# Kernel optimization log

Measured on AMD Instinct MI355X. Metric: run time of the kernel, lower is better.

Reference implementation:

```python
import jax, jax.numpy as jnp
import numpy as np

B, S, E, H = 2, 2048, 1024, 16
DH = E // H


def setup_inputs() -> dict:
    key = jax.random.key(0)
    ks = jax.random.split(key, 9)
    s = 1.0 / np.sqrt(E)
    return {
        "queries": jax.random.normal(ks[0], (B, S, E), dtype=jnp.float32),
        "keys": jax.random.normal(ks[1], (B, S, E), dtype=jnp.float32),
        "values": jax.random.normal(ks[2], (B, S, E), dtype=jnp.float32),
        "mask": jax.random.randint(ks[3], (B, 1, 1, S), 0, 2, dtype=jnp.int32),
        "Wq": jax.random.normal(ks[4], (E, E), dtype=jnp.float32) * s,
        "Wk": jax.random.normal(ks[5], (E, E), dtype=jnp.float32) * s,
        "Wv": jax.random.normal(ks[6], (E, E), dtype=jnp.float32) * s,
        "Wo": jax.random.normal(ks[7], (E, E), dtype=jnp.float32) * s,
        "bo": jax.random.normal(ks[8], (E,), dtype=jnp.float32) * s,
    }


def reference(queries, keys, values, mask, Wq, Wk, Wv, Wo, bo):
    n, d_q, _ = queries.shape
    d_k = keys.shape[1]
    # Linear projections (torch Linear: x @ W.T), then split into heads
    q = (queries @ Wq.T).reshape(n, d_q, H, DH)
    k = (keys @ Wk.T).reshape(n, d_k, H, DH)
    v = (values @ Wv.T).reshape(n, d_k, H, DH)
    # [n, H, d_q, d_k] attention scores
    energy = jnp.einsum("nqhd,nkhd->nhqk", q, k)
    energy = jnp.where(mask == 0, jnp.float32(-1e20), energy)
    # NOTE: original scales by sqrt(key seq length), not head dim -- kept faithful
    attn = jax.nn.softmax(energy / jnp.sqrt(jnp.float32(d_k)), axis=3)
    out = jnp.einsum("nhql,nlhd->nqhd", attn, v).reshape(n, d_q, E)
    return out @ Wo.T + bo
```

## Files before the change

kernel.cpp:

```cpp
#include <hip/hip_runtime.h>
#include <hip/hip_bf16.h>

#define BB 2
#define SS 2048
#define EE 1024
#define HH 16
#define DHH 64

using bf16x8 = __attribute__((ext_vector_type(8))) __bf16;
using f32x4  = __attribute__((ext_vector_type(4))) float;

#if __has_builtin(__builtin_amdgcn_exp2f)
#define EXP2(x) __builtin_amdgcn_exp2f(x)
#else
#define EXP2(x) __exp2f(x)
#endif

static __device__ __forceinline__ unsigned short f2bf(float f) {
    unsigned int u = __float_as_uint(f);
    u += 0x7FFFu + ((u >> 16) & 1u);
    return (unsigned short)(u >> 16);
}

static __device__ __forceinline__ unsigned int pk2bf(float lo, float hi) {
    union { __hip_bfloat162 h2; unsigned int u; } c;
    c.h2 = __float22bfloat162_rn(float2{lo, hi});
    return c.u;
}

static __device__ __forceinline__ void async_load16(const void* g, void* l) {
    __builtin_amdgcn_global_load_lds(
        (const __attribute__((address_space(1))) unsigned int*)g,
        (__attribute__((address_space(3))) unsigned int*)l, 16, 0, 0);
}

__global__ void cvt_kernel(const float* __restrict__ W0, const float* __restrict__ W1,
                           const float* __restrict__ W2, const float* __restrict__ W3,
                           const float* __restrict__ X0, const float* __restrict__ X1,
                           const float* __restrict__ X2,
                           unsigned short* __restrict__ Wb,
                           unsigned short* __restrict__ D0, unsigned short* __restrict__ D1,
                           unsigned short* __restrict__ D2)
{
    const int z = blockIdx.y;
    const float* src;
    unsigned short* dst;
    if (z < 4) {
        if (blockIdx.x >= 512) return;
        src = (z == 0) ? W0 : (z == 1) ? W1 : (z == 2) ? W2 : W3;
        dst = Wb + (size_t)z * 1048576;
    } else {
        src = (z == 4) ? X0 : (z == 5) ? X1 : X2;
        dst = (z == 4) ? D0 : (z == 5) ? D1 : D2;
    }
    const size_t base = (size_t)blockIdx.x * 2048 + (size_t)threadIdx.x * 8;
    const float4 f0 = *(const float4*)(src + base);
    const float4 f1 = *(const float4*)(src + base + 4);
    uint4 p;
    p.x = pk2bf(f0.x, f0.y); p.y = pk2bf(f0.z, f0.w);
    p.z = pk2bf(f1.x, f1.y); p.w = pk2bf(f1.z, f1.w);
    *(uint4*)(dst + base) = p;
}

template<int MT, int NT, bool BF16OUT>
__global__ __launch_bounds__(256, 3)
void gemm_xwt(const unsigned short* __restrict__ X0, const unsigned short* __restrict__ X1,
              const unsigned short* __restrict__ X2,
              const unsigned short* __restrict__ W0, const unsigned short* __restrict__ W1,
              const unsigned short* __restrict__ W2,
              void* __restrict__ Y0, void* __restrict__ Y1, void* __restrict__ Y2,
              const float* __restrict__ bias, int M, int N, int K,
              float s0, float s1, float s2)
{
    constexpr int BK = 32;
    constexpr int NI = MT / 32;
    constexpr int NJ = NT / 32;
    __shared__ __align__(16) unsigned short As[2][MT * BK];
    __shared__ __align__(16) unsigned short Bs[2][NT * BK];

    const int z = blockIdx.z;
    const unsigned short* __restrict__ X = (z == 0) ? X0 : ((z == 1) ? X1 : X2);
    const unsigned short* __restrict__ W = (z == 0) ? W0 : ((z == 1) ? W1 : W2);
    void* __restrict__ Y                 = (z == 0) ? Y0 : ((z == 1) ? Y1 : Y2);
    const float ysc                      = (z == 0) ? s0 : ((z == 1) ? s1 : s2);

    const int tid  = threadIdx.x;
    const int lane = tid & 63;
    const int wave = tid >> 6;
    const int wm   = (wave >> 1) * (MT / 2);
    const int wn   = (wave & 1) * (NT / 2);
    const int m0   = blockIdx.y * MT;
    const int n0   = blockIdx.x * NT;
    const int l16  = lane & 15;
    const int quad = lane >> 4;

    const int arow = lane >> 2;
    const int akc  = (lane & 3) * 8;

    f32x4 acc[NI][NJ];
    #pragma unroll
    for (int i = 0; i < NI; i++)
        #pragma unroll
        for (int j = 0; j < NJ; j++) acc[i][j] = f32x4{0.f, 0.f, 0.f, 0.f};

    auto stage = [&](int k0, int buf) {
        #pragma unroll
        for (int j = 0; j < NT / 64; j++) {
            const int rr = wave * (NT / 4) + j * 16;
            async_load16(W + (size_t)(n0 + rr + arow) * K + k0 + akc, Bs[buf] + rr * BK);
        }
        #pragma unroll
        for (int j = 0; j < MT / 64; j++) {
            const int rr = wave * (MT / 4) + j * 16;
            async_load16(X + (size_t)(m0 + rr + arow) * K + k0 + akc, As[buf] + rr * BK);
        }
    };

    stage(0, 0);
    const int niter = K / BK;
    for (int i = 0; i < niter; i++) {
        const int cur = i & 1;
        __syncthreads();
        if (i + 1 < niter) stage((i + 1) * BK, cur ^ 1);

        bf16x8 afrag[NI], bfrag[NJ];
        #pragma unroll
        for (int ii = 0; ii < NI; ii++)
            afrag[ii] = *(const bf16x8*)(As[cur] + (wm + ii * 16 + l16) * BK + quad * 8);
        #pragma unroll
        for (int j = 0; j < NJ; j++)
            bfrag[j] = *(const bf16x8*)(Bs[cur] + (wn + j * 16 + l16) * BK + quad * 8);
        #pragma unroll
        for (int ii = 0; ii < NI; ii++)
            #pragma unroll
            for (int j = 0; j < NJ; j++)
                acc[ii][j] = __builtin_amdgcn_mfma_f32_16x16x32_bf16(afrag[ii], bfrag[j], acc[ii][j], 0, 0, 0);
    }

    #pragma unroll
    for (int i = 0; i < NI; i++) {
        #pragma unroll
        for (int j = 0; j < NJ; j++) {
            #pragma unroll
            for (int r = 0; r < 4; r++) {
                const int row = m0 + wm + i * 16 + quad * 4 + r;
                const int col = n0 + wn + j * 16 + l16;
                const float v = acc[i][j][r];
                if (BF16OUT) {
                    ((unsigned short*)Y)[(size_t)row * N + col] = f2bf(v * ysc);
                } else {
                    ((float*)Y)[(size_t)row * N + col] = v + bias[col];
                }
            }
        }
    }
}

__global__ __launch_bounds__(256, 1)
void compact_kernel(const unsigned short* __restrict__ Kb,
                    const unsigned short* __restrict__ Vb,
                    const int* __restrict__ mask,
                    unsigned short* __restrict__ Kc,
                    unsigned short* __restrict__ Vtc)
{
    constexpr int LDE = 264;
    __shared__ int srcIdx[64];
    __shared__ int wsum[4];
    __shared__ __align__(16) unsigned short T[64 * LDE];

    const int tid  = threadIdx.x;
    const int lane = tid & 63;
    const int wave = tid >> 6;
    const int b    = blockIdx.y;
    const int t0   = blockIdx.x * 64;

    const int base = tid * 8;
    int v[8]; int run = 0;
    #pragma unroll
    for (int i = 0; i < 8; i++) { v[i] = (mask[b * SS + base + i] != 0) ? 1 : 0; run += v[i]; }

    int inc = run;
    #pragma unroll
    for (int d = 1; d < 64; d <<= 1) {
        int n = __shfl_up(inc, d, 64);
        if (lane >= d) inc += n;
    }
    if (lane == 63) wsum[wave] = inc;
    __syncthreads();
    const int nkeep = wsum[0] + wsum[1] + wsum[2] + wsum[3];
    if (t0 >= nkeep) return;

    if (tid < 64) srcIdx[tid] = -1;
    __syncthreads();

    int r = inc - run;
    #pragma unroll
    for (int w = 0; w < 4; w++) if (w < wave) r += wsum[w];
    #pragma unroll
    for (int i = 0; i < 8; i++) {
        if (v[i]) {
            if (r >= t0 && r < t0 + 64) srcIdx[r - t0] = base + i;
            r++;
        }
    }
    __syncthreads();

    {
        const int j = tid >> 2, part = tid & 3;
        const int s = srcIdx[j];
        uint4* dst = (uint4*)(Kc + ((size_t)(b * SS + t0 + j)) * EE + part * 256);
        if (s >= 0) {
            const uint4* src = (const uint4*)(Kb + ((size_t)(b * SS + s)) * EE + part * 256);
            #pragma unroll
            for (int c = 0; c < 32; c++) dst[c] = src[c];
        } else {
            #pragma unroll
            for (int c = 0; c < 32; c++) dst[c] = uint4{0, 0, 0, 0};
        }
    }

    for (int ec = 0; ec < 4; ec++) {
        __syncthreads();
        {
            const int j = tid >> 2, part = tid & 3;
            const int s = srcIdx[j];
            uint4* trow = (uint4*)(T + j * LDE + part * 64);
            if (s >= 0) {
                const uint4* src = (const uint4*)(Vb + ((size_t)(b * SS + s)) * EE + ec * 256 + part * 64);
                #pragma unroll
                for (int c = 0; c < 8; c++) trow[c] = src[c];
            } else {
                #pragma unroll
                for (int c = 0; c < 8; c++) trow[c] = uint4{0, 0, 0, 0};
            }
        }
        __syncthreads();
        {
            const int e = ec * 256 + tid;
            unsigned short* drow = Vtc + ((size_t)(b * EE + e)) * SS + t0;
            unsigned short tmp[64];
            #pragma unroll
            for (int j2 = 0; j2 < 64; j2++) tmp[j2] = T[j2 * LDE + tid];
            #pragma unroll
            for (int c = 0; c < 8; c++) ((uint4*)drow)[c] = ((const uint4*)tmp)[c];
        }
    }
}

__global__ __launch_bounds__(256, 2)
void attn_kernel(const unsigned short* __restrict__ Qb,
                 const unsigned short* __restrict__ Kc,
                 const unsigned short* __restrict__ Vtc,
                 const int* __restrict__ mask,
                 unsigned short* __restrict__ AO)
{
    constexpr int LDK = 68;
    constexpr int LDV = 68;
    constexpr int LDP = 68;
    __shared__ __align__(16) unsigned short Ks[64 * LDK];
    __shared__ __align__(16) unsigned short Vs[64 * LDV];
    __shared__ __align__(16) unsigned short Ps[4 * 32 * LDP];
    __shared__ __align__(16) float Msf[64];
    __shared__ int nk_s;

    const int tid  = threadIdx.x;
    const int lane = tid & 63;
    const int wave = tid >> 6;
    const int l16  = lane & 15;
    const int quad = lane >> 4;

    const int linear = blockIdx.x;
    const int bh     = (linear & 7) * 4 + ((linear >> 3) & 3);
    const int qblk   = linear >> 5;
    const int b  = bh >> 4;
    const int h  = bh & 15;
    const int q0 = qblk * 128 + wave * 32;

    if (tid == 0) nk_s = 0;
    __syncthreads();
    {
        int cnt = 0;
        #pragma unroll
        for (int i = 0; i < 8; i++) cnt += (mask[b * SS + tid * 8 + i] != 0) ? 1 : 0;
        #pragma unroll
        for (int d = 32; d >= 1; d >>= 1) cnt += __shfl_xor(cnt, d, 64);
        if (lane == 0) atomicAdd(&nk_s, cnt);
    }
    __syncthreads();
    const int nkeep  = nk_s;
    const int ntiles = (nkeep + 63) >> 6;

    bf16x8 qf[2][2];
    #pragma unroll
    for (int g = 0; g < 2; g++) {
        const unsigned short* qptr = Qb + (size_t)(b * SS + q0 + g * 16 + l16) * EE + h * DHH;
        qf[g][0] = *(const bf16x8*)(qptr + quad * 8);
        qf[g][1] = *(const bf16x8*)(qptr + 32 + quad * 8);
    }

    float lsum[2] = {0.f, 0.f};
    f32x4 o_acc[2][4];
    #pragma unroll
    for (int g = 0; g < 2; g++)
        #pragma unroll
        for (int j = 0; j < 4; j++) o_acc[g][j] = f32x4{0.f, 0.f, 0.f, 0.f};

    unsigned short* Pw = Ps + wave * 32 * LDP;

    const int srow = tid >> 2;
    const int sc   = (tid & 3) * 16;

    uint4 kr0, kr1, vr0, vr1;
    auto gload = [&](int t0) {
        const unsigned short* kg = Kc + (size_t)(b * SS + t0 + srow) * EE + h * DHH + sc;
        kr0 = *(const uint4*)(kg);
        kr1 = *(const uint4*)(kg + 8);
        const unsigned short* vg = Vtc + (size_t)(b * EE + h * DHH + srow) * SS + t0 + sc;
        vr0 = *(const uint4*)(vg);
        vr1 = *(const uint4*)(vg + 8);
    };
    gload(0);

    for (int it = 0; it < ntiles; it++) {
        const int t0 = it * 64;
        __syncthreads();
        *(uint4*)(Ks + srow * LDK + sc)     = kr0;
        *(uint4*)(Ks + srow * LDK + sc + 8) = kr1;
        *(uint4*)(Vs + srow * LDV + sc)     = vr0;
        *(uint4*)(Vs + srow * LDV + sc + 8) = vr1;
        if (tid < 64) Msf[tid] = (t0 + tid < nkeep) ? 0.0f : -150.0f;
        __syncthreads();

        if (it + 1 < ntiles) gload(t0 + 64);

        #pragma unroll
        for (int nt = 0; nt < 4; nt++) {
            bf16x8 kf0 = *(const bf16x8*)(Ks + (nt * 16 + l16) * LDK + quad * 8);
            bf16x8 kf1 = *(const bf16x8*)(Ks + (nt * 16 + l16) * LDK + 32 + quad * 8);
            const f32x4 cinit = *(const f32x4*)(Msf + nt * 16 + quad * 4);
            #pragma unroll
            for (int g = 0; g < 2; g++) {
                f32x4 a = __builtin_amdgcn_mfma_f32_16x16x32_bf16(kf0, qf[g][0], cinit, 0, 0, 0);
                a = __builtin_amdgcn_mfma_f32_16x16x32_bf16(kf1, qf[g][1], a, 0, 0, 0);
                const float p0 = EXP2(a[0]);
                const float p1 = EXP2(a[1]);
                const float p2 = EXP2(a[2]);
                const float p3 = EXP2(a[3]);
                lsum[g] += (p0 + p1) + (p2 + p3);
                uint2 pck;
                pck.x = pk2bf(p0, p1);
                pck.y = pk2bf(p2, p3);
                *(uint2*)(Pw + (g * 16 + l16) * LDP + nt * 16 + quad * 4) = pck;
            }
        }

        __builtin_amdgcn_s_waitcnt(0xC07F);

        #pragma unroll
        for (int s2 = 0; s2 < 2; s2++) {
            bf16x8 pf0 = *(const bf16x8*)(Pw + l16 * LDP + s2 * 32 + quad * 8);
            bf16x8 pf1 = *(const bf16x8*)(Pw + (16 + l16) * LDP + s2 * 32 + quad * 8);
            #pragma unroll
            for (int jg = 0; jg < 4; jg++) {
                bf16x8 vf = *(const bf16x8*)(Vs + (jg * 16 + l16) * LDV + s2 * 32 + quad * 8);
                o_acc[0][jg] = __builtin_amdgcn_mfma_f32_16x16x32_bf16(vf, pf0, o_acc[0][jg], 0, 0, 0);
                o_acc[1][jg] = __builtin_amdgcn_mfma_f32_16x16x32_bf16(vf, pf1, o_acc[1][jg], 0, 0, 0);
            }
        }
    }

    #pragma unroll
    for (int g = 0; g < 2; g++) {
        float ls = lsum[g];
        ls += __shfl_xor(ls, 16, 64);
        ls += __shfl_xor(ls, 32, 64);
        const float rl = 1.0f / ls;
        const size_t orow = (size_t)(b * SS + q0 + g * 16 + l16) * EE + h * DHH;
        #pragma unroll
        for (int jg = 0; jg < 4; jg++) {
            uint2 pck;
            pck.x = pk2bf(o_acc[g][jg][0] * rl, o_acc[g][jg][1] * rl);
            pck.y = pk2bf(o_acc[g][jg][2] * rl, o_acc[g][jg][3] * rl);
            *(uint2*)(AO + orow + jg * 16 + quad * 4) = pck;
        }
    }
}

extern "C" void kernel_launch(void* const* d_in, const int* in_sizes, int n_in,
                              void* d_out, int out_size, void* d_ws, size_t ws_size,
                              hipStream_t stream)
{
    (void)in_sizes; (void)n_in; (void)out_size; (void)ws_size;
    const float* queries = (const float*)d_in[0];
    const float* keys    = (const float*)d_in[1];
    const float* values  = (const float*)d_in[2];
    const int*   mask    = (const int*)d_in[3];
    const float* Wq      = (const float*)d_in[4];
    const float* Wk      = (const float*)d_in[5];
    const float* Wv      = (const float*)d_in[6];
    const float* Wo      = (const float*)d_in[7];
    const float* bo      = (const float*)d_in[8];

    const size_t NE = (size_t)BB * SS * EE;
    const size_t WE = (size_t)EE * EE;

    unsigned short* Xq  = (unsigned short*)d_out;
    unsigned short* Xk  = Xq + NE;
    unsigned short* Kc  = (unsigned short*)d_out;
    unsigned short* Vtc = Kc + NE;
    unsigned short* Wb  = (unsigned short*)d_ws;
    unsigned short* Xv  = Wb + 4 * WE;
    unsigned short* Qb  = Xv + NE;
    unsigned short* Kb  = Qb + NE;
    unsigned short* Vb  = Kb + NE;
    unsigned short* AOb = Xv;

    const int M = BB * SS, N = EE, K = EE;
    const float qscale = 0.022097086912079608f * 1.4426950408889634f;

    cvt_kernel<<<dim3(2048, 7), 256, 0, stream>>>(
        Wq, Wk, Wv, Wo, queries, keys, values, Wb, Xq, Xk, Xv);

    dim3 gproj(N / 128, M / 128, 3);
    gemm_xwt<128, 128, true><<<gproj, 256, 0, stream>>>(
        Xq, Xk, Xv, Wb, Wb + WE, Wb + 2 * WE,
        (void*)Qb, (void*)Kb, (void*)Vb, nullptr, M, N, K,
        qscale, 1.0f, 1.0f);

    compact_kernel<<<dim3(SS / 64, BB), 256, 0, stream>>>(Kb, Vb, mask, Kc, Vtc);

    attn_kernel<<<dim3(512), 256, 0, stream>>>(Qb, Kc, Vtc, mask, AOb);

    dim3 gout(N / 64, M / 64, 1);
    gemm_xwt<64, 64, false><<<gout, 256, 0, stream>>>(
        AOb, AOb, AOb, Wb + 3 * WE, Wb + 3 * WE, Wb + 3 * WE,
        d_out, d_out, d_out, bo, M, N, K, 1.0f, 1.0f, 1.0f);
}
```

Measured before the change: 236.3 us.

## Use 32x32x16 MFMA in attention with register-level P transpose via permlane32_swap

Rewrites the attention inner loop to use 32x32x16 bf16 MFMA tiles instead of 16x16x32. The softmax probabilities are moved between lanes with permlane32_swap rather than staged through a shared-memory P buffer, and wave priority is raised around the MFMA sections. Masking now zeroes probabilities only on the partial tile instead of adding a bias. The aim is to cut LDS traffic and the count of MFMA issues. The epilogue now writes scalar bf16 values using per-row reciprocals held in LDS, which may lower store efficiency.

```diff
diff --git a/kernel.cpp b/kernel.cpp
--- a/kernel.cpp
+++ b/kernel.cpp
@@ -9,6 +9,8 @@
 
 using bf16x8 = __attribute__((ext_vector_type(8))) __bf16;
 using f32x4  = __attribute__((ext_vector_type(4))) float;
+using f32x16 = __attribute__((ext_vector_type(16))) float;
+using uint2v = __attribute__((ext_vector_type(2))) unsigned int;
 
 #if __has_builtin(__builtin_amdgcn_exp2f)
 #define EXP2(x) __builtin_amdgcn_exp2f(x)
@@ -256,18 +258,16 @@
 {
     constexpr int LDK = 68;
     constexpr int LDV = 68;
-    constexpr int LDP = 68;
     __shared__ __align__(16) unsigned short Ks[64 * LDK];
     __shared__ __align__(16) unsigned short Vs[64 * LDV];
-    __shared__ __align__(16) unsigned short Ps[4 * 32 * LDP];
-    __shared__ __align__(16) float Msf[64];
+    __shared__ float Lsum[4][32];
     __shared__ int nk_s;
 
     const int tid  = threadIdx.x;
     const int lane = tid & 63;
     const int wave = tid >> 6;
-    const int l16  = lane & 15;
-    const int quad = lane >> 4;
+    const int l32  = lane & 31;
+    const int hi   = lane >> 5;
 
     const int linear = blockIdx.x;
     const int bh     = (linear & 7) * 4 + ((linear >> 3) & 3);
@@ -290,22 +290,19 @@
     const int nkeep  = nk_s;
     const int ntiles = (nkeep + 63) >> 6;
 
-    bf16x8 qf[2][2];
-    #pragma unroll
-    for (int g = 0; g < 2; g++) {
-        const unsigned short* qptr = Qb + (size_t)(b * SS + q0 + g * 16 + l16) * EE + h * DHH;
-        qf[g][0] = *(const bf16x8*)(qptr + quad * 8);
-        qf[g][1] = *(const bf16x8*)(qptr + 32 + quad * 8);
-    }
-
-    float lsum[2] = {0.f, 0.f};
-    f32x4 o_acc[2][4];
-    #pragma unroll
-    for (int g = 0; g < 2; g++)
-        #pragma unroll
-        for (int j = 0; j < 4; j++) o_acc[g][j] = f32x4{0.f, 0.f, 0.f, 0.f};
-
-    unsigned short* Pw = Ps + wave * 32 * LDP;
+    bf16x8 qf[4];
+    {
+        const unsigned short* qptr = Qb + (size_t)(b * SS + q0 + l32) * EE + h * DHH + hi * 8;
+        #pragma unroll
+        for (int t = 0; t < 4; t++) qf[t] = *(const bf16x8*)(qptr + t * 16);
+    }
+
+    float lsum = 0.f;
+    f32x16 o_acc[2];
+    #pragma unroll
+    for (int d = 0; d < 2; d++)
+        #pragma unroll
+        for (int r = 0; r < 16; r++) o_acc[d][r] = 0.f;
 
     const int srow = tid >> 2;
     const int sc   = (tid & 3) * 16;
@@ -328,61 +325,88 @@
         *(uint4*)(Ks + srow * LDK + sc + 8) = kr1;
         *(uint4*)(Vs + srow * LDV + sc)     = vr0;
         *(uint4*)(Vs + srow * LDV + sc + 8) = vr1;
-        if (tid < 64) Msf[tid] = (t0 + tid < nkeep) ? 0.0f : -150.0f;
         __syncthreads();
 
         if (it + 1 < ntiles) gload(t0 + 64);
 
-        #pragma unroll
-        for (int nt = 0; nt < 4; nt++) {
-            bf16x8 kf0 = *(const bf16x8*)(Ks + (nt * 16 + l16) * LDK + quad * 8);
-            bf16x8 kf1 = *(const bf16x8*)(Ks + (nt * 16 + l16) * LDK + 32 + quad * 8);
-            const f32x4 cinit = *(const f32x4*)(Msf + nt * 16 + quad * 4);
-            #pragma unroll
-            for (int g = 0; g < 2; g++) {
-                f32x4 a = __builtin_amdgcn_mfma_f32_16x16x32_bf16(kf0, qf[g][0], cinit, 0, 0, 0);
-                a = __builtin_amdgcn_mfma_f32_16x16x32_bf16(kf1, qf[g][1], a, 0, 0, 0);
-                const float p0 = EXP2(a[0]);
-                const float p1 = EXP2(a[1]);
-                const float p2 = EXP2(a[2]);
-                const float p3 = EXP2(a[3]);
-                lsum[g] += (p0 + p1) + (p2 + p3);
-                uint2 pck;
-                pck.x = pk2bf(p0, p1);
-                pck.y = pk2bf(p2, p3);
-                *(uint2*)(Pw + (g * 16 + l16) * LDP + nt * 16 + quad * 4) = pck;
-            }
-        }
-
-        __builtin_amdgcn_s_waitcnt(0xC07F);
-
-        #pragma unroll
-        for (int s2 = 0; s2 < 2; s2++) {
-            bf16x8 pf0 = *(const bf16x8*)(Pw + l16 * LDP + s2 * 32 + quad * 8);
-            bf16x8 pf1 = *(const bf16x8*)(Pw + (16 + l16) * LDP + s2 * 32 + quad * 8);
-            #pragma unroll
-            for (int jg = 0; jg < 4; jg++) {
-                bf16x8 vf = *(const bf16x8*)(Vs + (jg * 16 + l16) * LDV + s2 * 32 + quad * 8);
-                o_acc[0][jg] = __builtin_amdgcn_mfma_f32_16x16x32_bf16(vf, pf0, o_acc[0][jg], 0, 0, 0);
-                o_acc[1][jg] = __builtin_amdgcn_mfma_f32_16x16x32_bf16(vf, pf1, o_acc[1][jg], 0, 0, 0);
-            }
-        }
-    }
-
-    #pragma unroll
-    for (int g = 0; g < 2; g++) {
-        float ls = lsum[g];
-        ls += __shfl_xor(ls, 16, 64);
+        const bool full = (t0 + 64 <= nkeep);
+
+        #pragma unroll
+        for (int blk = 0; blk < 2; blk++) {
+            f32x16 s;
+            __builtin_amdgcn_s_setprio(1);
+            {
+                bf16x8 kf = *(const bf16x8*)(Ks + (blk * 32 + l32) * LDK + hi * 8);
+                f32x16 z;
+                #pragma unroll
+                for (int r = 0; r < 16; r++) z[r] = 0.f;
+                s = __builtin_amdgcn_mfma_f32_32x32x16_bf16(kf, qf[0], z, 0, 0, 0);
+            }
+            #pragma unroll
+            for (int t = 1; t < 4; t++) {
+                bf16x8 kf = *(const bf16x8*)(Ks + (blk * 32 + l32) * LDK + t * 16 + hi * 8);
+                s = __builtin_amdgcn_mfma_f32_32x32x16_bf16(kf, qf[t], s, 0, 0, 0);
+            }
+            __builtin_amdgcn_s_setprio(0);
+
+            float p[16];
+            #pragma unroll
+            for (int r = 0; r < 16; r++) p[r] = EXP2(s[r]);
+            if (!full) {
+                const int keyb = t0 + blk * 32 + 4 * hi;
+                #pragma unroll
+                for (int r = 0; r < 16; r++)
+                    if (keyb + ((r & 3) + 8 * (r >> 2)) >= nkeep) p[r] = 0.f;
+            }
+            #pragma unroll
+            for (int r = 0; r < 16; r += 4)
+                lsum += ((p[r] + p[r + 1]) + (p[r + 2] + p[r + 3]));
+
+            const unsigned int u0 = pk2bf(p[0],  p[1]);
+            const unsigned int u1 = pk2bf(p[2],  p[3]);
+            const unsigned int u2 = pk2bf(p[4],  p[5]);
+            const unsigned int u3 = pk2bf(p[6],  p[7]);
+            const unsigned int u4 = pk2bf(p[8],  p[9]);
+            const unsigned int u5 = pk2bf(p[10], p[11]);
+            const unsigned int u6 = pk2bf(p[12], p[13]);
+            const unsigned int u7 = pk2bf(p[14], p[15]);
+            const uint2v s02 = __builtin_amdgcn_permlane32_swap(u0, u2, false, false);
+            const uint2v s13 = __builtin_amdgcn_permlane32_swap(u1, u3, false, false);
+            const uint2v s46 = __builtin_amdgcn_permlane32_swap(u4, u6, false, false);
+            const uint2v s57 = __builtin_amdgcn_permlane32_swap(u5, u7, false, false);
+
+            union { unsigned int u[4]; bf16x8 v; } pa0, pa1;
+            pa0.u[0] = s02.x; pa0.u[1] = s13.x; pa0.u[2] = s02.y; pa0.u[3] = s13.y;
+            pa1.u[0] = s46.x; pa1.u[1] = s57.x; pa1.u[2] = s46.y; pa1.u[3] = s57.y;
+
+            __builtin_amdgcn_s_setprio(1);
+            #pragma unroll
+            for (int kc = 0; kc < 2; kc++) {
+                const bf16x8 pav = (kc == 0) ? pa0.v : pa1.v;
+                #pragma unroll
+                for (int dblk = 0; dblk < 2; dblk++) {
+                    bf16x8 vf = *(const bf16x8*)(Vs + (dblk * 32 + l32) * LDV + blk * 32 + kc * 16 + hi * 8);
+                    o_acc[dblk] = __builtin_amdgcn_mfma_f32_32x32x16_bf16(pav, vf, o_acc[dblk], 0, 0, 0);
+                }
+            }
+            __builtin_amdgcn_s_setprio(0);
+        }
+    }
+
+    {
+        float ls = lsum;
         ls += __shfl_xor(ls, 32, 64);
-        const float rl = 1.0f / ls;
-        const size_t orow = (size_t)(b * SS + q0 + g * 16 + l16) * EE + h * DHH;
-        #pragma unroll
-        for (int jg = 0; jg < 4; jg++) {
-            uint2 pck;
-            pck.x = pk2bf(o_acc[g][jg][0] * rl, o_acc[g][jg][1] * rl);
-            pck.y = pk2bf(o_acc[g][jg][2] * rl, o_acc[g][jg][3] * rl);
-            *(uint2*)(AO + orow + jg * 16 + quad * 4) = pck;
-        }
+        Lsum[wave][l32] = 1.0f / ls;
+    }
+    __builtin_amdgcn_s_waitcnt(0xC07F);
+
+    #pragma unroll
+    for (int r = 0; r < 16; r++) {
+        const int qr = (r & 3) + 8 * (r >> 2) + 4 * hi;
+        const float rl = Lsum[wave][qr];
+        const size_t orow = (size_t)(b * SS + q0 + qr) * EE + h * DHH + l32;
+        AO[orow]      = f2bf(o_acc[0][r] * rl);
+        AO[orow + 32] = f2bf(o_acc[1][r] * rl);
     }
 }
 
```

Result: faster. 221.6 us (-6.2%).
